# Kernel tuning notes

Measured on AMD Instinct MI355X. Metric: run time of the kernel, lower is better.

Reference implementation:

```python
import jax, jax.numpy as jnp
import numpy as np

MAX_POS = 8192
SOFT_CAP = 5.0


def rms_norm(x, scale, eps=1e-6):
    # RMSBatchNorm approximated as RMS normalization over channels with learned scale
    return x * jax.lax.rsqrt(jnp.mean(x * x, axis=-1, keepdims=True) + eps) * scale


def layer_norm(x, scale, offset, eps=1e-5):
    mean = jnp.mean(x, axis=-1, keepdims=True)
    var = jnp.mean(jnp.square(x - mean), axis=-1, keepdims=True)
    return (x - mean) * jax.lax.rsqrt(var + eps) * scale + offset


def apply_rope(x, max_position=MAX_POS):
    # x: [B, S, H, C]
    B, S, H, C = x.shape
    positions = jnp.arange(S, dtype=x.dtype).reshape(1, S)
    num_freq = C // 2
    inv_freq = (1.0 / (jnp.arange(num_freq) + jnp.geomspace(1, max_position - num_freq + 1, num_freq))).astype(x.dtype)
    theta = jnp.einsum('bs,f->bsf', positions, inv_freq)
    theta = jnp.repeat(theta, 2, axis=-1)[..., None, :]  # [1, S, 1, C]
    x_rotated = jnp.stack([-x[..., 1::2], x[..., ::2]], axis=-1).reshape(x.shape)
    return x * jnp.cos(theta) + x_rotated * jnp.sin(theta)


def setup_inputs() -> dict:
    key = jax.random.key(0)
    ks = jax.random.split(key, 16)
    B, S, D = 2, 2048, 1536
    H, CQK, CV = 8, 128, 192
    inp = {
        'x': jax.random.normal(ks[0], (B, S, D), jnp.float32),
        'attention_bias': jax.random.normal(ks[1], (B, H, S, S), jnp.float32),
        'rms_in_scale': jnp.ones((D,), jnp.float32),
        'wq': jax.random.normal(ks[2], (D, H * CQK), jnp.float32) / np.sqrt(D),
        'wk': jax.random.normal(ks[3], (D, CQK), jnp.float32) / np.sqrt(D),
        'wv': jax.random.normal(ks[4], (D, CV), jnp.float32) / np.sqrt(D),
        'q_scale': jnp.ones((CQK,), jnp.float32),
        'q_offset': jnp.zeros((CQK,), jnp.float32),
        'k_scale': jnp.ones((CQK,), jnp.float32),
        'k_offset': jnp.zeros((CQK,), jnp.float32),
        'v_scale': jnp.ones((CV,), jnp.float32),
        'v_offset': jnp.zeros((CV,), jnp.float32),
        'wo': jax.random.normal(ks[5], (H * CV, D), jnp.float32) / np.sqrt(H * CV),
        'bo': jnp.zeros((D,), jnp.float32),
        'rms_out_scale': jnp.ones((D,), jnp.float32),
    }
    return inp


def reference(x, attention_bias, rms_in_scale, wq, wk, wv, q_scale, q_offset,
              k_scale, k_offset, v_scale, v_offset, wo, bo, rms_out_scale):
    B, S, D = x.shape
    H, CQK, CV = 8, 128, 192
    h = rms_norm(x, rms_in_scale)
    q = layer_norm((h @ wq).reshape(B, S, H, CQK), q_scale, q_offset)
    k = layer_norm((h @ wk).reshape(B, S, 1, CQK), k_scale, k_offset)
    v = layer_norm((h @ wv).reshape(B, S, 1, CV), v_scale, v_offset)
    q = apply_rope(q)
    k = apply_rope(k)
    # MQA logits: single shared K head
    logits = jnp.einsum('bshc,bSc->bhsS', q, k[:, :, 0], preferred_element_type=jnp.float32)
    logits = logits / np.sqrt(128.0)
    logits = (logits + attention_bias).astype(jnp.float32)
    logits = jnp.tanh(logits / SOFT_CAP) * SOFT_CAP
    weights = jax.nn.softmax(logits, axis=-1)
    y = jnp.einsum('bhsS,bSc->bshc', weights, v[:, :, 0]).astype(q.dtype)
    y = y.reshape(B, S, H * CV) @ wo + bo
    return rms_norm(y, rms_out_scale)
```

## Files before the change

### kernel.cpp

```cpp
#include <hip/hip_runtime.h>
#include <hip/hip_bf16.h>

typedef unsigned short u16;
typedef short bf16x8 __attribute__((ext_vector_type(8)));
typedef float f32x4 __attribute__((ext_vector_type(4)));

#define NB 2
#define NS 2048
#define ND 1536
#define NH 8
#define NCQK 128
#define NCV 192
#define NBS 4096
#define NPAD 1408

__device__ __forceinline__ float bf2f(u16 u) {
  unsigned v = ((unsigned)u) << 16;
  return __builtin_bit_cast(float, v);
}
__device__ __forceinline__ u16 f2bf(float f) {
  unsigned u = __builtin_bit_cast(unsigned, f);
  u += 0x7fffu + ((u >> 16) & 1u);
  return (u16)(u >> 16);
}
__device__ __forceinline__ f32x4 mfma16(bf16x8 a, bf16x8 b, f32x4 c) {
  return __builtin_amdgcn_mfma_f32_16x16x32_bf16(a, b, c, 0, 0, 0);
}

__global__ void transpose_k(const float* __restrict__ in, u16* __restrict__ out,
                            int K, int N) {
  __shared__ float t[64][65];
  const int n0 = blockIdx.x * 64, k0 = blockIdx.y * 64;
  const int tid = threadIdx.x;
  const int rl = tid >> 4, cl = (tid & 15) * 4;
  for (int p = 0; p < 4; p++) {
    int k = rl + p * 16;
    float4 v = *(const float4*)(in + (size_t)(k0 + k) * N + n0 + cl);
    t[k][cl] = v.x; t[k][cl + 1] = v.y; t[k][cl + 2] = v.z; t[k][cl + 3] = v.w;
  }
  __syncthreads();
  const int rn = tid >> 3, ck = (tid & 7) * 8;
  for (int p = 0; p < 2; p++) {
    int n = rn + p * 32;
    u16 tmp[8];
    for (int j = 0; j < 8; j++) tmp[j] = f2bf(t[ck + j][n]);
    *(uint4*)(out + (size_t)(n0 + n) * K + k0 + ck) = *(uint4*)tmp;
  }
}

__global__ void rmsnorm_in_k(const float* __restrict__ x, const float* __restrict__ scale,
                             u16* __restrict__ h) {
  __shared__ float sbuf[4];
  const int row = blockIdx.x, tid = threadIdx.x;
  const float* xr = x + (size_t)row * ND;
  float v[6]; float ss = 0.f;
  for (int i = 0; i < 6; i++) { v[i] = xr[tid + i * 256]; ss += v[i] * v[i]; }
  for (int o = 32; o; o >>= 1) ss += __shfl_xor(ss, o);
  if ((tid & 63) == 0) sbuf[tid >> 6] = ss;
  __syncthreads();
  ss = sbuf[0] + sbuf[1] + sbuf[2] + sbuf[3];
  const float inv = rsqrtf(ss * (1.f / ND) + 1e-6f);
  u16* hr = h + (size_t)row * ND;
  for (int i = 0; i < 6; i++) {
    int c = tid + i * 256;
    hr[c] = f2bf(v[i] * inv * scale[c]);
  }
}

template <bool F32OUT>
__global__ __launch_bounds__(256, 2)
void gemm_nt(const u16* __restrict__ A, const u16* __restrict__ Bt,
             float* __restrict__ Cf, u16* __restrict__ Cb, int M, int N, int K) {
  __shared__ __align__(16) u16 As[128 * 64];
  __shared__ __align__(16) u16 Bs[128 * 64];
  const int tid = threadIdx.x;
  const int wave = tid >> 6, lane = tid & 63, quad = lane >> 4, l16 = lane & 15;
  const int m0 = blockIdx.y * 128, n0 = blockIdx.x * 128;
  const int mrb = (wave & 1) * 4, nrb = (wave >> 1) * 4;
  f32x4 acc[4][4] = {};
  for (int k0 = 0; k0 < K; k0 += 64) {
    if (k0) __syncthreads();
    for (int i = 0; i < 4; i++) {
      int g = wave * 4 + i;
      int rb = g >> 1, kh = g & 1;
      int row = rb * 16 + l16, kc = kh * 4 + quad;
      uint4 va = *(const uint4*)(A + (size_t)(m0 + row) * K + k0 + kc * 8);
      uint4 vb = *(const uint4*)(Bt + (size_t)(n0 + row) * K + k0 + kc * 8);
      *(uint4*)&As[(rb * 8 + kh * 4) * 128 + lane * 8] = va;
      *(uint4*)&Bs[(rb * 8 + kh * 4) * 128 + lane * 8] = vb;
    }
    __syncthreads();
    for (int kk = 0; kk < 2; kk++) {
      bf16x8 af[4], bfr[4];
      for (int f = 0; f < 4; f++)
        af[f] = *(const bf16x8*)&As[(((mrb + f) * 8 + kk * 4 + quad) * 16 + l16) * 8];
      for (int f = 0; f < 4; f++)
        bfr[f] = *(const bf16x8*)&Bs[(((nrb + f) * 8 + kk * 4 + quad) * 16 + l16) * 8];
      for (int mf = 0; mf < 4; mf++)
        for (int nf = 0; nf < 4; nf++)
          acc[mf][nf] = mfma16(af[mf], bfr[nf], acc[mf][nf]);
    }
  }
  for (int mf = 0; mf < 4; mf++)
    for (int nf = 0; nf < 4; nf++)
      for (int r = 0; r < 4; r++) {
        int m = m0 + (wave & 1) * 64 + mf * 16 + quad * 4 + r;
        int n = n0 + (wave >> 1) * 64 + nf * 16 + l16;
        if (F32OUT) Cf[(size_t)m * N + n] = acc[mf][nf][r];
        else        Cb[(size_t)m * N + n] = f2bf(acc[mf][nf][r]);
      }
}

__global__ void ln_rope_k(const float* __restrict__ qkv,
                          const float* __restrict__ qs, const float* __restrict__ qo,
                          const float* __restrict__ ks, const float* __restrict__ ko,
                          const float* __restrict__ vs, const float* __restrict__ vo,
                          u16* __restrict__ Qg, u16* __restrict__ Kg, u16* __restrict__ Vg) {
  const int row = blockIdx.x;
  const int b = row >> 11, s = row & (NS - 1);
  const int wave = threadIdx.x >> 6, lane = threadIdx.x & 63;
  const float* base = qkv + (size_t)row * NPAD;
  const float gsp = __expf(logf(8129.f) * ((float)lane * (1.f / 63.f)));
  const float invf = 1.f / ((float)lane + gsp);
  float sn, cs;
  sincosf((float)s * invf, &sn, &cs);

  for (int hh = 0; hh < 2; hh++) {
    const int h = wave * 2 + hh;
    const float* p = base + h * NCQK;
    float x0 = p[lane * 2], x1 = p[lane * 2 + 1];
    float s1 = x0 + x1, s2 = x0 * x0 + x1 * x1;
    for (int o = 32; o; o >>= 1) { s1 += __shfl_xor(s1, o); s2 += __shfl_xor(s2, o); }
    float mean = s1 * (1.f / NCQK);
    float inv = rsqrtf(s2 * (1.f / NCQK) - mean * mean + 1e-5f);
    float y0 = (x0 - mean) * inv * qs[lane * 2] + qo[lane * 2];
    float y1 = (x1 - mean) * inv * qs[lane * 2 + 1] + qo[lane * 2 + 1];
    u16* dst = Qg + (size_t)row * (NH * NCQK) + h * NCQK + lane * 2;
    dst[0] = f2bf(y0 * cs - y1 * sn);
    dst[1] = f2bf(y1 * cs + y0 * sn);
  }
  if (wave == 0) {
    const float* p = base + NH * NCQK;
    float x0 = p[lane * 2], x1 = p[lane * 2 + 1];
    float s1 = x0 + x1, s2 = x0 * x0 + x1 * x1;
    for (int o = 32; o; o >>= 1) { s1 += __shfl_xor(s1, o); s2 += __shfl_xor(s2, o); }
    float mean = s1 * (1.f / NCQK);
    float inv = rsqrtf(s2 * (1.f / NCQK) - mean * mean + 1e-5f);
    float y0 = (x0 - mean) * inv * ks[lane * 2] + ko[lane * 2];
    float y1 = (x1 - mean) * inv * ks[lane * 2 + 1] + ko[lane * 2 + 1];
    u16* dst = Kg + (size_t)row * NCQK + lane * 2;
    dst[0] = f2bf(y0 * cs - y1 * sn);
    dst[1] = f2bf(y1 * cs + y0 * sn);
  }
  if (wave == 1) {
    const float* p = base + NH * NCQK + NCQK;
    float x[3]; float s1 = 0.f, s2 = 0.f;
    for (int i = 0; i < 3; i++) { x[i] = p[lane + i * 64]; s1 += x[i]; s2 += x[i] * x[i]; }
    for (int o = 32; o; o >>= 1) { s1 += __shfl_xor(s1, o); s2 += __shfl_xor(s2, o); }
    float mean = s1 * (1.f / NCV);
    float inv = rsqrtf(s2 * (1.f / NCV) - mean * mean + 1e-5f);
    for (int i = 0; i < 3; i++) {
      int c = lane + i * 64;
      float y = (x[i] - mean) * inv * vs[c] + vo[c];
      Vg[(size_t)(b * NCV + c) * NS + s] = f2bf(y);
    }
  }
}

__global__ __launch_bounds__(256, 2)
void attn_k(const u16* __restrict__ Qg, const u16* __restrict__ Kg,
            const u16* __restrict__ Vg, const float* __restrict__ bias,
            u16* __restrict__ Y) {
  __shared__ __align__(16) u16 Qs[64 * 128];
  __shared__ __align__(16) u16 Ks[64 * 128];
  __shared__ __align__(16) u16 Vs[192 * 64];
  __shared__ __align__(16) u16 Ps[64 * 64];
  const int tid = threadIdx.x;
  const int wave = tid >> 6, lane = tid & 63, quad = lane >> 4, l16 = lane & 15;
  const int s0 = blockIdx.x * 64;
  const int h = blockIdx.y, b = blockIdx.z;

  for (int i = 0; i < 4; i++) {
    int g = wave * 4 + i;
    int qb = g >> 2, kcg = g & 3;
    int q = qb * 16 + l16, kc = kcg * 4 + quad;
    uint4 v = *(const uint4*)(Qg + ((size_t)((b * NS + s0 + q) * NH + h)) * NCQK + kc * 8);
    *(uint4*)&Qs[(qb * 16 + kcg * 4) * 128 + lane * 8] = v;
  }

  f32x4 oacc[12] = {};
  float lsum[4] = {0.f, 0.f, 0.f, 0.f};
  bf16x8 qa[4];
  const float* brow = bias + ((size_t)(b * NH + h) * NS + s0 + wave * 16) * NS;

  for (int kt = 0; kt < NS / 64; kt++) {
    const int key0 = kt * 64;
    if (kt) __syncthreads();
    for (int i = 0; i < 4; i++) {
      int g = wave * 4 + i;
      int kb = g >> 2, kcg = g & 3;
      int ky = kb * 16 + l16, kc = kcg * 4 + quad;
      uint4 v = *(const uint4*)(Kg + (size_t)(b * NS + key0 + ky) * NCQK + kc * 8);
      *(uint4*)&Ks[(kb * 16 + kcg * 4) * 128 + lane * 8] = v;
    }
    for (int i = 0; i < 6; i++) {
      int g = wave * 6 + i;
      int cb = g >> 1, kh = g & 1;
      int cv = cb * 16 + l16, kc = kh * 4 + quad;
      uint4 v = *(const uint4*)(Vg + (size_t)(b * NCV + cv) * NS + key0 + kc * 8);
      *(uint4*)&Vs[(cb * 8 + kh * 4) * 128 + lane * 8] = v;
    }
    __syncthreads();
    if (kt == 0)
      for (int kk = 0; kk < 4; kk++)
        qa[kk] = *(const bf16x8*)&Qs[((wave * 16 + kk * 4 + quad) * 16 + l16) * 8];

    f32x4 sacc[4] = {};
    for (int kk = 0; kk < 4; kk++)
      for (int nb = 0; nb < 4; nb++) {
        bf16x8 kf = *(const bf16x8*)&Ks[((nb * 16 + kk * 4 + quad) * 16 + l16) * 8];
        sacc[nb] = mfma16(qa[kk], kf, sacc[nb]);
      }

    for (int nb = 0; nb < 4; nb++) {
      const int key_l = nb * 16 + l16;
      const float* bp = brow + key0 + key_l;
      for (int r = 0; r < 4; r++) {
        const int qrow = quad * 4 + r;
        float sv = sacc[nb][r] * 0.08838834764831845f + bp[(size_t)qrow * NS];
        float e2 = __expf(sv * 0.4f);
        float cap = 5.f - 10.f / (e2 + 1.f);
        u16 pb = f2bf(__expf(cap));
        lsum[r] += bf2f(pb);
        Ps[((wave * 8 + (key_l >> 3)) * 16 + qrow) * 8 + (key_l & 7)] = pb;
      }
    }

    for (int kk = 0; kk < 2; kk++) {
      bf16x8 pa = *(const bf16x8*)&Ps[((wave * 8 + kk * 4 + quad) * 16 + l16) * 8];
      for (int nb = 0; nb < 12; nb++) {
        bf16x8 vf = *(const bf16x8*)&Vs[((nb * 8 + kk * 4 + quad) * 16 + l16) * 8];
        oacc[nb] = mfma16(pa, vf, oacc[nb]);
      }
    }
  }

  for (int r = 0; r < 4; r++)
    for (int o = 1; o < 16; o <<= 1) lsum[r] += __shfl_xor(lsum[r], o);
  for (int r = 0; r < 4; r++) {
    const float inv = 1.f / lsum[r];
    const int m = s0 + wave * 16 + quad * 4 + r;
    u16* yr = Y + (size_t)(b * NS + m) * ND + h * NCV;
    for (int nb = 0; nb < 12; nb++) yr[nb * 16 + l16] = f2bf(oacc[nb][r] * inv);
  }
}

__global__ void final_k(const u16* __restrict__ yo, const float* __restrict__ bo,
                        const float* __restrict__ scale, float* __restrict__ out) {
  __shared__ float sbuf[4];
  const int row = blockIdx.x, tid = threadIdx.x;
  const u16* yr = yo + (size_t)row * ND;
  float v[6]; float ss = 0.f;
  for (int i = 0; i < 6; i++) {
    int c = tid + i * 256;
    v[i] = bf2f(yr[c]) + bo[c];
    ss += v[i] * v[i];
  }
  for (int o = 32; o; o >>= 1) ss += __shfl_xor(ss, o);
  if ((tid & 63) == 0) sbuf[tid >> 6] = ss;
  __syncthreads();
  ss = sbuf[0] + sbuf[1] + sbuf[2] + sbuf[3];
  const float inv = rsqrtf(ss * (1.f / ND) + 1e-6f);
  float* orow = out + (size_t)row * ND;
  for (int i = 0; i < 6; i++) {
    int c = tid + i * 256;
    orow[c] = v[i] * inv * scale[c];
  }
}

extern "C" void kernel_launch(void* const* d_in, const int* in_sizes, int n_in,
                              void* d_out, int out_size, void* d_ws, size_t ws_size,
                              hipStream_t stream) {
  const float* x    = (const float*)d_in[0];
  const float* bias = (const float*)d_in[1];
  const float* rin  = (const float*)d_in[2];
  const float* wq   = (const float*)d_in[3];
  const float* wk   = (const float*)d_in[4];
  const float* wv   = (const float*)d_in[5];
  const float* qsc  = (const float*)d_in[6];
  const float* qof  = (const float*)d_in[7];
  const float* ksc  = (const float*)d_in[8];
  const float* kof  = (const float*)d_in[9];
  const float* vsc  = (const float*)d_in[10];
  const float* vof  = (const float*)d_in[11];
  const float* wo   = (const float*)d_in[12];
  const float* bo   = (const float*)d_in[13];
  const float* rout = (const float*)d_in[14];

  char* ws = (char*)d_ws;
  size_t off = 0;
  auto alloc = [&](size_t bytes) -> void* {
    void* p = ws + off;
    off += (bytes + 255) & ~(size_t)255;
    return p;
  };
  u16*   h    = (u16*)alloc((size_t)NBS * ND * 2);
  u16*   wtq  = (u16*)alloc((size_t)NPAD * ND * 2);
  u16*   wto  = (u16*)alloc((size_t)ND * ND * 2);
  float* qkv  = (float*)alloc((size_t)NBS * NPAD * 4);
  u16*   Qb   = (u16*)alloc((size_t)NBS * NH * NCQK * 2);
  u16*   Kb   = (u16*)alloc((size_t)NBS * NCQK * 2);
  u16*   Vtb  = (u16*)alloc((size_t)NB * NCV * NS * 2);
  u16*   Ybf  = (u16*)alloc((size_t)NBS * ND * 2);
  u16*   Yob  = (u16*)alloc((size_t)NBS * ND * 2);

  transpose_k<<<dim3(16, 24), 256, 0, stream>>>(wq, wtq, ND, 1024);
  transpose_k<<<dim3(2, 24), 256, 0, stream>>>(wk, wtq + (size_t)1024 * ND, ND, 128);
  transpose_k<<<dim3(3, 24), 256, 0, stream>>>(wv, wtq + (size_t)1152 * ND, ND, 192);
  transpose_k<<<dim3(24, 24), 256, 0, stream>>>(wo, wto, ND, ND);
  rmsnorm_in_k<<<NBS, 256, 0, stream>>>(x, rin, h);
  gemm_nt<true><<<dim3(NPAD / 128, NBS / 128), 256, 0, stream>>>(h, wtq, qkv, nullptr, NBS, NPAD, ND);
  ln_rope_k<<<NBS, 256, 0, stream>>>(qkv, qsc, qof, ksc, kof, vsc, vof, Qb, Kb, Vtb);
  attn_k<<<dim3(NS / 64, NH, NB), 256, 0, stream>>>(Qb, Kb, Vtb, bias, Ybf);
  gemm_nt<false><<<dim3(ND / 128, NBS / 128), 256, 0, stream>>>(Ybf, wto, nullptr, Yob, NBS, ND, ND);
  final_k<<<NBS, 256, 0, stream>>>(Yob, bo, rout, (float*)d_out);
}
```

Baseline: 629.3 us.

## Use direct global-to-LDS loads and prefetch bias into registers in attention

Replaces the register round-trip global loads with global_load_lds builtins for the GEMM and attention tiles (Q, K, V). The attention kernel now issues the next tile's bias loads into registers and reloads K/V at the end of each iteration, so bias latency can overlap with the store and barrier. The goal is to cut VGPR pressure and the latency of the strided fp32 bias reads, which dominate attention traffic. It keeps a single LDS buffer with two barriers per iteration, so K/V loads still do not overlap with compute, and it relies on the LDS layout matching the builtin's per-lane write order.

Measured after the change: 592.9 us. 5.8% less time.

```diff
diff --git a/kernel.cpp b/kernel.cpp
--- a/kernel.cpp
+++ b/kernel.cpp
@@ -22,6 +22,11 @@
   unsigned u = __builtin_bit_cast(unsigned, f);
   u += 0x7fffu + ((u >> 16) & 1u);
   return (u16)(u >> 16);
+}
+__device__ __forceinline__ void glds16(const u16* g, u16* l) {
+  __builtin_amdgcn_global_load_lds(
+      (const __attribute__((address_space(1))) void*)g,
+      (__attribute__((address_space(3))) void*)l, 16, 0, 0);
 }
 __device__ __forceinline__ f32x4 mfma16(bf16x8 a, bf16x8 b, f32x4 c) {
   return __builtin_amdgcn_mfma_f32_16x16x32_bf16(a, b, c, 0, 0, 0);
@@ -84,10 +89,8 @@
       int g = wave * 4 + i;
       int rb = g >> 1, kh = g & 1;
       int row = rb * 16 + l16, kc = kh * 4 + quad;
-      uint4 va = *(const uint4*)(A + (size_t)(m0 + row) * K + k0 + kc * 8);
-      uint4 vb = *(const uint4*)(Bt + (size_t)(n0 + row) * K + k0 + kc * 8);
-      *(uint4*)&As[(rb * 8 + kh * 4) * 128 + lane * 8] = va;
-      *(uint4*)&Bs[(rb * 8 + kh * 4) * 128 + lane * 8] = vb;
+      glds16(A + (size_t)(m0 + row) * K + k0 + kc * 8, &As[(rb * 8 + kh * 4) * 128]);
+      glds16(Bt + (size_t)(n0 + row) * K + k0 + kc * 8, &Bs[(rb * 8 + kh * 4) * 128]);
     }
     __syncthreads();
     for (int kk = 0; kk < 2; kk++) {
@@ -180,41 +183,36 @@
   const int s0 = blockIdx.x * 64;
   const int h = blockIdx.y, b = blockIdx.z;
 
+  const u16* Kbase = Kg + (size_t)(b * NS) * NCQK;
+  const u16* Vbase = Vg + (size_t)(b * NCV) * NS;
+  const float* brow = bias + ((size_t)(b * NH + h) * NS + s0 + wave * 16) * NS;
+
   for (int i = 0; i < 4; i++) {
-    int g = wave * 4 + i;
-    int qb = g >> 2, kcg = g & 3;
-    int q = qb * 16 + l16, kc = kcg * 4 + quad;
-    uint4 v = *(const uint4*)(Qg + ((size_t)((b * NS + s0 + q) * NH + h)) * NCQK + kc * 8);
-    *(uint4*)&Qs[(qb * 16 + kcg * 4) * 128 + lane * 8] = v;
-  }
+    glds16(Qg + ((size_t)((b * NS + s0 + wave * 16 + l16) * NH + h)) * NCQK + (i * 4 + quad) * 8,
+           &Qs[(wave * 16 + i * 4) * 128]);
+    glds16(Kbase + (size_t)(wave * 16 + l16) * NCQK + (i * 4 + quad) * 8,
+           &Ks[(wave * 16 + i * 4) * 128]);
+  }
+  for (int i = 0; i < 6; i++) {
+    int g = wave * 6 + i;
+    int cb = g >> 1, kh = g & 1;
+    glds16(Vbase + (size_t)(cb * 16 + l16) * NS + (kh * 4 + quad) * 8,
+           &Vs[(cb * 8 + kh * 4) * 128]);
+  }
+  float breg[16];
+  for (int nb = 0; nb < 4; nb++)
+    for (int r = 0; r < 4; r++)
+      breg[nb * 4 + r] = brow[(size_t)(quad * 4 + r) * NS + nb * 16 + l16];
+  __syncthreads();
+
+  bf16x8 qa[4];
+  for (int kk = 0; kk < 4; kk++)
+    qa[kk] = *(const bf16x8*)&Qs[((wave * 16 + kk * 4 + quad) * 16 + l16) * 8];
 
   f32x4 oacc[12] = {};
   float lsum[4] = {0.f, 0.f, 0.f, 0.f};
-  bf16x8 qa[4];
-  const float* brow = bias + ((size_t)(b * NH + h) * NS + s0 + wave * 16) * NS;
 
   for (int kt = 0; kt < NS / 64; kt++) {
-    const int key0 = kt * 64;
-    if (kt) __syncthreads();
-    for (int i = 0; i < 4; i++) {
-      int g = wave * 4 + i;
-      int kb = g >> 2, kcg = g & 3;
-      int ky = kb * 16 + l16, kc = kcg * 4 + quad;
-      uint4 v = *(const uint4*)(Kg + (size_t)(b * NS + key0 + ky) * NCQK + kc * 8);
-      *(uint4*)&Ks[(kb * 16 + kcg * 4) * 128 + lane * 8] = v;
-    }
-    for (int i = 0; i < 6; i++) {
-      int g = wave * 6 + i;
-      int cb = g >> 1, kh = g & 1;
-      int cv = cb * 16 + l16, kc = kh * 4 + quad;
-      uint4 v = *(const uint4*)(Vg + (size_t)(b * NCV + cv) * NS + key0 + kc * 8);
-      *(uint4*)&Vs[(cb * 8 + kh * 4) * 128 + lane * 8] = v;
-    }
-    __syncthreads();
-    if (kt == 0)
-      for (int kk = 0; kk < 4; kk++)
-        qa[kk] = *(const bf16x8*)&Qs[((wave * 16 + kk * 4 + quad) * 16 + l16) * 8];
-
     f32x4 sacc[4] = {};
     for (int kk = 0; kk < 4; kk++)
       for (int nb = 0; nb < 4; nb++) {
@@ -224,10 +222,9 @@
 
     for (int nb = 0; nb < 4; nb++) {
       const int key_l = nb * 16 + l16;
-      const float* bp = brow + key0 + key_l;
       for (int r = 0; r < 4; r++) {
         const int qrow = quad * 4 + r;
-        float sv = sacc[nb][r] * 0.08838834764831845f + bp[(size_t)qrow * NS];
+        float sv = sacc[nb][r] * 0.08838834764831845f + breg[nb * 4 + r];
         float e2 = __expf(sv * 0.4f);
         float cap = 5.f - 10.f / (e2 + 1.f);
         u16 pb = f2bf(__expf(cap));
@@ -242,6 +239,24 @@
         bf16x8 vf = *(const bf16x8*)&Vs[((nb * 8 + kk * 4 + quad) * 16 + l16) * 8];
         oacc[nb] = mfma16(pa, vf, oacc[nb]);
       }
+    }
+
+    if (kt + 1 < NS / 64) {
+      const int key0 = (kt + 1) * 64;
+      for (int nb = 0; nb < 4; nb++)
+        for (int r = 0; r < 4; r++)
+          breg[nb * 4 + r] = brow[(size_t)(quad * 4 + r) * NS + key0 + nb * 16 + l16];
+      __syncthreads();
+      for (int i = 0; i < 4; i++)
+        glds16(Kbase + (size_t)(key0 + wave * 16 + l16) * NCQK + (i * 4 + quad) * 8,
+               &Ks[(wave * 16 + i * 4) * 128]);
+      for (int i = 0; i < 6; i++) {
+        int g = wave * 6 + i;
+        int cb = g >> 1, kh = g & 1;
+        glds16(Vbase + (size_t)(cb * 16 + l16) * NS + key0 + (kh * 4 + quad) * 8,
+               &Vs[(cb * 8 + kh * 4) * 128]);
+      }
+      __syncthreads();
     }
   }
 
```
